# Kernel optimization log

Hardware: AMD Instinct MI355X
Metric: run time of the kernel (lower is better)

The kernel has to match this reference:

```python
import jax, jax.numpy as jnp
import numpy as np

NUM_EXPERTS = 8
TOP_K = 2
IN_C, HID, OUT_C, R_C = 192, 384, 192, 8
B, H, W = 4, 128, 128


def setup_inputs() -> dict:
    key = jax.random.key(0)
    ks = jax.random.split(key, 12)
    s = 0.05
    return {
        "x": jax.random.normal(ks[0], (B, IN_C, H, W), jnp.float32),
        "router_input": jax.random.normal(ks[1], (B, R_C, H, W), jnp.float32),
        "router_W": jax.random.normal(ks[2], (NUM_EXPERTS, R_C), jnp.float32) * s,
        "router_b": jnp.zeros((NUM_EXPERTS,), jnp.float32),
        "W1": jax.random.normal(ks[3], (NUM_EXPERTS, HID, IN_C), jnp.float32) * s,
        "b1": jnp.zeros((NUM_EXPERTS, HID), jnp.float32),
        "W2": jax.random.normal(ks[4], (NUM_EXPERTS, HID, HID), jnp.float32) * s,
        "b2": jnp.zeros((NUM_EXPERTS, HID), jnp.float32),
        "W3": jax.random.normal(ks[5], (NUM_EXPERTS, OUT_C, HID), jnp.float32) * (s * 0.1),
        "b3": jnp.zeros((NUM_EXPERTS, OUT_C), jnp.float32),
    }


def _gates(router_input, router_W, router_b):
    # logits: (B, E, H, W) via 1x1 conv == per-pixel linear
    logits = jnp.einsum('ec,bchw->behw', router_W, router_input) + router_b[None, :, None, None]
    lt = jnp.moveaxis(logits, 1, -1)                      # (B,H,W,E)
    _, idx = jax.lax.top_k(lt, TOP_K)                     # (B,H,W,K)
    onehot = jax.nn.one_hot(idx, NUM_EXPERTS, dtype=bool).any(axis=-2)  # (B,H,W,E)
    masked = jnp.where(onehot, lt, -jnp.inf)
    gates = jax.nn.softmax(masked, axis=-1)               # (B,H,W,E)
    return jnp.moveaxis(gates, -1, 1)                     # (B,E,H,W)


def reference(x, router_input, router_W, router_b, W1, b1, W2, b2, W3, b3):
    gates = _gates(router_input, router_W, router_b)      # (B,E,H,W)
    out = jnp.zeros((x.shape[0], OUT_C) + x.shape[2:], x.dtype)
    gelu = lambda t: jax.nn.gelu(t, approximate=False)    # torch nn.GELU is exact
    for e in range(NUM_EXPERTS):
        h1 = gelu(jnp.einsum('oc,bchw->bohw', W1[e], x) + b1[e][None, :, None, None])
        h2 = gelu(jnp.einsum('oc,bchw->bohw', W2[e], h1) + b2[e][None, :, None, None])
        y = jnp.einsum('oc,bchw->bohw', W3[e], h2) + b3[e][None, :, None, None]
        out = out + gates[:, e:e + 1] * y
    return out
```

## Files before the change

### kernel.cpp

```cpp
#include <hip/hip_runtime.h>
#include <math.h>

#define NE 8
#define IN_C 192
#define HID 384
#define OUT_C 192
#define R_C 8
#define HW 16384
#define NPIX 65536
#define PPB 16384
#define TNP 128

typedef _Float16 h8_t __attribute__((ext_vector_type(8)));
typedef float f32x4 __attribute__((ext_vector_type(4)));

__device__ __forceinline__ float gelu_exact(float v) {
  float z  = v * 0.70710678118654752f;
  float az = fabsf(z);
  float t  = __builtin_amdgcn_rcpf(1.0f + 0.3275911f * az);
  float p  = ((((1.061405429f * t - 1.453152027f) * t + 1.421413741f) * t
               - 0.284496736f) * t + 0.254829592f) * t;
  float er = 1.0f - p * __expf(-z * z);
  er = copysignf(er, z);
  return 0.5f * v * (1.0f + er);
}

__global__ __launch_bounds__(256) void router_kernel(
    const float* __restrict__ rin, const float* __restrict__ rW,
    const float* __restrict__ rb, int* __restrict__ counts,
    int* __restrict__ lists, float* __restrict__ gatev) {
  const int tid = threadIdx.x;
  const int pid = blockIdx.x * 256 + tid;
  const int img = pid >> 14;
  const int p = pid & (PPB - 1);

  __shared__ int lcount[NE];
  __shared__ int lbase[NE];
  if (tid < NE) lcount[tid] = 0;
  __syncthreads();

  const float* rbase = rin + (size_t)img * R_C * HW + p;
  float r[R_C];
#pragma unroll
  for (int c = 0; c < R_C; ++c) r[c] = rbase[(size_t)c * HW];
  float lg[NE];
#pragma unroll
  for (int e = 0; e < NE; ++e) {
    float s = rb[e];
#pragma unroll
    for (int c = 0; c < R_C; ++c) s += rW[e * R_C + c] * r[c];
    lg[e] = s;
  }
  int e0 = 0; float l0 = lg[0];
#pragma unroll
  for (int e = 1; e < NE; ++e) { if (lg[e] > l0) { l0 = lg[e]; e0 = e; } }
  int e1 = -1; float l1 = -3.4e38f;
#pragma unroll
  for (int e = 0; e < NE; ++e) {
    if (e != e0 && lg[e] > l1) { l1 = lg[e]; e1 = e; }
  }
  float ex  = expf(l1 - l0);
  float inv = 1.0f / (1.0f + ex);
  float g0 = inv, g1 = ex * inv;

  int pos0 = atomicAdd(&lcount[e0], 1);
  int pos1 = atomicAdd(&lcount[e1], 1);
  __syncthreads();
  if (tid < NE) lbase[tid] = atomicAdd(&counts[tid * 4 + img], lcount[tid]);
  __syncthreads();

  int i0 = (e0 * 4 + img) * PPB + lbase[e0] + pos0;
  lists[i0] = p;
  gatev[i0] = g0;
  int i1 = (e1 * 4 + img) * PPB + lbase[e1] + pos1;
  lists[i1] = p | (1 << 14);
  gatev[i1] = g1;
}

__global__ __launch_bounds__(256) void cvt_blob(
    const float* __restrict__ W1, const float* __restrict__ W2,
    const float* __restrict__ W3, _Float16* __restrict__ Wb) {
  int t = blockIdx.x * 256 + threadIdx.x;
  if (t >= NE * 73728) return;
  int e = t / 73728, r = t % 73728;
  int cg = r / 1536, w = r % 1536;
  int j4 = w & 1, gm = w >> 1;
  int m = gm % 192, g = gm / 192;
  const float* src; int row, col, lda;
  if (cg < 6)       { src = W1 + (size_t)e * 73728;  row = m;       col = 32 * cg + 8 * g + 4 * j4; lda = 192; }
  else if (cg < 18) { int s = cg - 6;  int c = s >> 1, mh = s & 1;
                      src = W2 + (size_t)e * 147456; row = 192 * mh + m; col = 32 * c + 8 * g + 4 * j4; lda = 384; }
  else if (cg < 24) { int c = cg - 18;
                      src = W1 + (size_t)e * 73728;  row = 192 + m; col = 32 * c + 8 * g + 4 * j4; lda = 192; }
  else if (cg < 36) { int s = cg - 24; int c = s >> 1, mh = s & 1;
                      src = W2 + (size_t)e * 147456; row = 192 * mh + m; col = 192 + 32 * c + 8 * g + 4 * j4; lda = 384; }
  else              { int c = cg - 36;
                      src = W3 + (size_t)e * 73728;  row = m;       col = 32 * c + 8 * g + 4 * j4; lda = 384; }
  float4 v = *(const float4*)(src + (size_t)row * lda + col);
  union { _Float16 h4[4]; uint2 u; } cv;
  cv.h4[0] = (_Float16)v.x; cv.h4[1] = (_Float16)v.y;
  cv.h4[2] = (_Float16)v.z; cv.h4[3] = (_Float16)v.w;
  ((uint2*)Wb)[t] = cv.u;
}

__global__ __launch_bounds__(256) void xt_kernel(const float* __restrict__ x,
                                                 _Float16* __restrict__ xt, int pair) {
  const int img2 = blockIdx.y;
  const float* xb = x + (size_t)(pair * 2 + img2) * IN_C * HW;
  _Float16* dst = xt + (size_t)img2 * PPB * 192;
  const int tid = threadIdx.x;
  const int p = blockIdx.x * 64 + (tid & 63);
  const int cq0 = tid >> 6;
#pragma unroll
  for (int cq = 0; cq < 6; ++cq) {
    int chq = cq * 4 + cq0;
    union { _Float16 h[8]; uint4 u; } pk;
#pragma unroll
    for (int j = 0; j < 8; ++j)
      pk.h[j] = (_Float16)xb[(size_t)(chq * 8 + j) * HW + p];
    *(uint4*)(dst + (size_t)p * 192 + chq * 8) = pk.u;
  }
}

struct Pipe {
  unsigned qi;
  int rslot;
  int cslot;
  const char* wq;
  char* RING;
  int tid, wid;
};

__device__ __forceinline__ void pipe_issue3(Pipe& P) {
#pragma unroll
  for (int k = 0; k < 3; ++k) {
    if (P.qi < 72) {
      __builtin_amdgcn_global_load_lds(
          (const __attribute__((address_space(1))) void*)(P.wq + P.tid * 16),
          (__attribute__((address_space(3))) void*)(P.RING + P.rslot * 8192 + P.wid * 1024),
          16, 0, 0);
      P.wq += 8192;
      P.qi++;
      P.rslot = (P.rslot == 5) ? 0 : P.rslot + 1;
    }
  }
}

__device__ __forceinline__ void mfma_chunk(const _Float16* __restrict__ A,
                                           const _Float16* __restrict__ B, int kb4,
                                           int m0, int nt0,
                                           f32x4 (&acc)[3][4], int lane) {
  const int l15 = lane & 15, g = lane >> 4;
  h8_t a[3], b[4];
#pragma unroll
  for (int i = 0; i < 3; ++i)
    a[i] = *(const h8_t*)(A + ((size_t)g * 192 + m0 + i * 16 + l15) * 8);
#pragma unroll
  for (int t = 0; t < 4; ++t)
    b[t] = *(const h8_t*)(B + (((size_t)(kb4 + g) * TNP) + (nt0 + t) * 16 + l15) * 8);
#pragma unroll
  for (int i = 0; i < 3; ++i)
#pragma unroll
    for (int t = 0; t < 4; ++t)
      acc[i][t] = __builtin_amdgcn_mfma_f32_16x16x32_f16(a[i], b[t], acc[i][t], 0, 0, 0);
}

template <bool LAST, bool DRAIN>
__device__ __forceinline__ void dphase(Pipe& P, const _Float16* __restrict__ Bsh,
                                       int kb0, int kb1,
                                       f32x4 (&accA)[3][4], f32x4 (&accB)[3][4],
                                       int m0loc, int nt0, int lane) {
  if (LAST)       asm volatile("s_waitcnt vmcnt(0)" ::: "memory");
  else if (DRAIN) asm volatile("s_waitcnt vmcnt(3) lgkmcnt(0)" ::: "memory");
  else            asm volatile("s_waitcnt vmcnt(3)" ::: "memory");
  __builtin_amdgcn_sched_barrier(0);
  __builtin_amdgcn_s_barrier();
  __builtin_amdgcn_sched_barrier(0);
  const _Float16* A0 = (const _Float16*)(P.RING + P.cslot * 12288);
  const _Float16* A1 = (const _Float16*)(P.RING + (P.cslot + 1) * 12288);
  __builtin_amdgcn_s_setprio(1);
  mfma_chunk(A0, Bsh, kb0, m0loc, nt0, accA, lane);
  mfma_chunk(A1, Bsh, kb1, m0loc, nt0, accB, lane);
  __builtin_amdgcn_s_setprio(0);
  P.cslot ^= 2;
  if (!LAST) {
    __builtin_amdgcn_sched_barrier(0);
    __builtin_amdgcn_s_barrier();
    __builtin_amdgcn_sched_barrier(0);
    pipe_issue3(P);
  }
}

__device__ __forceinline__ void act_store(f32x4 (&acc)[3][4], const float* __restrict__ bias,
                                          _Float16* __restrict__ Dst, int m0, int nt0, int lane) {
  const int l15 = lane & 15, g = lane >> 4;
#pragma unroll
  for (int i = 0; i < 3; ++i) {
    int rb = m0 + i * 16 + 4 * g;
    float4 bv = *(const float4*)(bias + rb);
#pragma unroll
    for (int t = 0; t < 4; ++t) {
      int n = (nt0 + t) * 16 + l15;
      union { _Float16 h[4]; uint2 u; } cv;
      cv.h[0] = (_Float16)gelu_exact(acc[i][t][0] + bv.x);
      cv.h[1] = (_Float16)gelu_exact(acc[i][t][1] + bv.y);
      cv.h[2] = (_Float16)gelu_exact(acc[i][t][2] + bv.z);
      cv.h[3] = (_Float16)gelu_exact(acc[i][t][3] + bv.w);
      *(uint2*)(Dst + (((size_t)(rb >> 3) * TNP) + n) * 8 + (rb & 7)) = cv.u;
    }
  }
}

__device__ __forceinline__ void ybuf_store(f32x4 (&acc)[3][4], const float* __restrict__ bias,
                                           _Float16* __restrict__ ybuf,
                                           const int* __restrict__ pidsl,
                                           const float* __restrict__ pg,
                                           int npt, int m0, int nt0, int lane) {
  const int l15 = lane & 15, g = lane >> 4;
#pragma unroll
  for (int t = 0; t < 4; ++t) {
    int n = (nt0 + t) * 16 + l15;
    if (n >= npt) continue;
    float gt = pg[n];
    _Float16* yb = ybuf + pidsl[n];
#pragma unroll
    for (int i = 0; i < 3; ++i) {
      int rb = m0 + i * 16 + 4 * g;
      float4 bv = *(const float4*)(bias + rb);
      union { _Float16 h[4]; uint2 u; } cv;
      cv.h[0] = (_Float16)((acc[i][t][0] + bv.x) * gt);
      cv.h[1] = (_Float16)((acc[i][t][1] + bv.y) * gt);
      cv.h[2] = (_Float16)((acc[i][t][2] + bv.z) * gt);
      cv.h[3] = (_Float16)((acc[i][t][3] + bv.w) * gt);
      *(uint2*)(yb + rb) = cv.u;
    }
  }
}

__global__ __launch_bounds__(512, 2) void moe_mfma_kernel(
    const _Float16* __restrict__ xt, const _Float16* __restrict__ Wb,
    const float* __restrict__ b1, const float* __restrict__ b2,
    const float* __restrict__ b3,
    const int* __restrict__ counts, const int* __restrict__ lists,
    const float* __restrict__ gatev, _Float16* __restrict__ ybuf, int pair) {
  const int e = blockIdx.x;
  const int img2 = blockIdx.y >> 7;
  const int tile = blockIdx.y & 127;
  const int img = pair * 2 + img2;
  const int cnt = counts[e * 4 + img];
  const int start = tile * TNP;
  if (start >= cnt) return;
  const int npt = min(TNP, cnt - start);

  __shared__ __align__(16) char smem[152832];
  _Float16* XB  = (_Float16*)smem;
  _Float16* H1a = (_Float16*)(smem + 49152);
  _Float16* H2  = (_Float16*)smem;
  char* RING   = smem + 98304;
  float* BIAS1 = (float*)(smem + 147456);
  float* BIAS2 = (float*)(smem + 148992);
  float* BIAS3 = (float*)(smem + 150528);
  int*   pp    = (int*)(smem + 151296);
  int*   pidsl = (int*)(smem + 151808);
  float* pg    = (float*)(smem + 152320);

  const int tid = threadIdx.x;
  const int lane = tid & 63;
  const int wid = tid >> 6;
  const int m0loc = (wid >> 1) * 48;
  const int nt0 = (wid & 1) * 4;

  if (tid < TNP) {
    int entry = 0; float g = 0.0f;
    if (tid < npt) {
      entry = lists[(e * 4 + img) * PPB + start + tid];
      g     = gatev[(e * 4 + img) * PPB + start + tid];
    }
    int p = entry & (PPB - 1);
    int slot = (entry >> 14) & 1;
    pp[tid] = img2 * PPB + p;
    pidsl[tid] = ((img2 * PPB + p) * 2 + slot) * 192;
    pg[tid] = g;
  }
  for (int i = tid; i < 960; i += 512) {
    if (i < 384) BIAS1[i] = b1[e * HID + i];
    else if (i < 768) BIAS2[i - 384] = b2[e * HID + (i - 384)];
    else BIAS3[i - 768] = b3[e * OUT_C + (i - 768)];
  }
  __syncthreads();

  for (int i = tid; i < 24 * TNP; i += 512) {
    int n = i & (TNP - 1);
    int c16 = i >> 7;
    uint4 v = {0, 0, 0, 0};
    if (n < npt) v = *(const uint4*)(xt + (size_t)pp[n] * 192 + c16 * 8);
    *(uint4*)(XB + ((size_t)c16 * TNP + n) * 8) = v;
  }
  __syncthreads();

  Pipe P{0u, 0, 0, (const char*)(Wb + (size_t)e * 294912), RING, tid, wid};
  pipe_issue3(P);
  pipe_issue3(P);

  f32x4 acc1[3][4], acc2a[3][4], acc2b[3][4];
#pragma unroll
  for (int i = 0; i < 3; ++i)
#pragma unroll
    for (int t = 0; t < 4; ++t) {
      acc1[i][t] = (f32x4){0.f, 0.f, 0.f, 0.f};
      acc2a[i][t] = (f32x4){0.f, 0.f, 0.f, 0.f};
      acc2b[i][t] = (f32x4){0.f, 0.f, 0.f, 0.f};
    }

#pragma unroll 1
  for (int s = 0; s < 3; ++s)
    dphase<false, false>(P, XB, 8 * s, 8 * s + 4, acc1, acc1, m0loc, nt0, lane);
  act_store(acc1, BIAS1, H1a, m0loc, nt0, lane);

  dphase<false, true>(P, H1a, 0, 0, acc2a, acc2b, m0loc, nt0, lane);
#pragma unroll 1
  for (int s = 1; s < 6; ++s)
    dphase<false, false>(P, H1a, 4 * s, 4 * s, acc2a, acc2b, m0loc, nt0, lane);

#pragma unroll
  for (int i = 0; i < 3; ++i)
#pragma unroll
    for (int t = 0; t < 4; ++t) acc1[i][t] = (f32x4){0.f, 0.f, 0.f, 0.f};
#pragma unroll 1
  for (int s = 0; s < 3; ++s)
    dphase<false, false>(P, XB, 8 * s, 8 * s + 4, acc1, acc1, m0loc, nt0, lane);
  act_store(acc1, BIAS1 + 192, H1a, m0loc, nt0, lane);

  dphase<false, true>(P, H1a, 0, 0, acc2a, acc2b, m0loc, nt0, lane);
#pragma unroll 1
  for (int s = 1; s < 6; ++s)
    dphase<false, false>(P, H1a, 4 * s, 4 * s, acc2a, acc2b, m0loc, nt0, lane);
  act_store(acc2a, BIAS2, H2, m0loc, nt0, lane);
  act_store(acc2b, BIAS2, H2, 192 + m0loc, nt0, lane);

#pragma unroll
  for (int i = 0; i < 3; ++i)
#pragma unroll
    for (int t = 0; t < 4; ++t) acc1[i][t] = (f32x4){0.f, 0.f, 0.f, 0.f};
  dphase<false, true>(P, H2, 0, 4, acc1, acc1, m0loc, nt0, lane);
#pragma unroll 1
  for (int s = 1; s < 5; ++s)
    dphase<false, false>(P, H2, 8 * s, 8 * s + 4, acc1, acc1, m0loc, nt0, lane);
  dphase<true, false>(P, H2, 40, 44, acc1, acc1, m0loc, nt0, lane);

  ybuf_store(acc1, BIAS3, ybuf, pidsl, pg, npt, m0loc, nt0, lane);
}

__global__ __launch_bounds__(256) void sum_kernel(
    const _Float16* __restrict__ ybuf, float* __restrict__ out, int pair) {
  __shared__ float ys[64][193];
  const int tid = threadIdx.x;
  const int img2 = blockIdx.x >> 8;
  const int p0 = (blockIdx.x & 255) * 64;
  const _Float16* yb = ybuf + (size_t)(img2 * PPB + p0) * 2 * 192;

  for (int t = tid; t < 64 * 48; t += 256) {
    int p = t / 48, c4 = t % 48;
    const uint2* y0 = (const uint2*)(yb + (size_t)p * 2 * 192) + c4;
    uint2 u0 = y0[0];
    uint2 u1 = y0[48];
    union { uint2 u; _Float16 h[4]; } a, b;
    a.u = u0; b.u = u1;
#pragma unroll
    for (int j = 0; j < 4; ++j)
      ys[p][c4 * 4 + j] = (float)a.h[j] + (float)b.h[j];
  }
  __syncthreads();

  float* ob = out + (size_t)(pair * 2 + img2) * OUT_C * HW + p0;
  for (int t = tid; t < OUT_C * 64; t += 256) {
    int c = t >> 6, p = t & 63;
    ob[(size_t)c * HW + p] = ys[p][c];
  }
}

extern "C" void kernel_launch(void* const* d_in, const int* in_sizes, int n_in,
                              void* d_out, int out_size, void* d_ws, size_t ws_size,
                              hipStream_t stream) {
  const float* x   = (const float*)d_in[0];
  const float* rin = (const float*)d_in[1];
  const float* rW  = (const float*)d_in[2];
  const float* rb  = (const float*)d_in[3];
  const float* W1  = (const float*)d_in[4];
  const float* b1  = (const float*)d_in[5];
  const float* W2  = (const float*)d_in[6];
  const float* b2  = (const float*)d_in[7];
  const float* W3  = (const float*)d_in[8];
  const float* b3  = (const float*)d_in[9];
  float* out = (float*)d_out;

  char* ws = (char*)d_ws;
  int*   counts = (int*)ws;
  int*   lists  = (int*)(ws + 1024);
  float* gatev  = (float*)(ws + 1024 + (size_t)NE * 4 * PPB * 4);
  _Float16* Wb  = (_Float16*)(ws + 1024 + 2 * (size_t)NE * 4 * PPB * 4);
  _Float16* ybuf = Wb + (size_t)NE * 294912;
  _Float16* xt = ybuf + (size_t)2 * PPB * 2 * 192;

  hipMemsetAsync(counts, 0, NE * 4 * sizeof(int), stream);

  cvt_blob<<<(NE * 73728 + 255) / 256, 256, 0, stream>>>(W1, W2, W3, Wb);

  router_kernel<<<NPIX / 256, 256, 0, stream>>>(rin, rW, rb, counts, lists, gatev);

  for (int pair = 0; pair < 2; ++pair) {
    xt_kernel<<<dim3(PPB / 64, 2), 256, 0, stream>>>(x, xt, pair);
    moe_mfma_kernel<<<dim3(NE, 256), 512, 0, stream>>>(
        xt, Wb, b1, b2, b3, counts, lists, gatev, ybuf, pair);
    sum_kernel<<<512, 256, 0, stream>>>(ybuf, out, pair);
  }
}
```

Measured before the change: 262.6 us.

## Halve pixel tile to 64 and use a double-buffered weight pipeline

The per-block pixel tile drops from 128 to 64, which halves shared memory (to about 78 KB) and the accumulator registers so more blocks fit per CU (launch bounds raised to 4). The 6-slot weight ring with 3-chunk issue is replaced by a simpler 2-slot double buffer of 12 KB chunks, with fully unrolled per-stage loops and explicit wait counts. The trade-off is that each weight chunk streamed from L2 is now reused across only half as many pixels, so weight traffic per pixel doubles, and the shallower prefetch depth leaves less latency hiding.

```diff
diff --git a/kernel.cpp b/kernel.cpp
--- a/kernel.cpp
+++ b/kernel.cpp
@@ -9,7 +9,7 @@
 #define HW 16384
 #define NPIX 65536
 #define PPB 16384
-#define TNP 128
+#define TNP 64
 
 typedef _Float16 h8_t __attribute__((ext_vector_type(8)));
 typedef float f32x4 __attribute__((ext_vector_type(4)));
@@ -122,76 +122,48 @@
   }
 }
 
-struct Pipe {
-  unsigned qi;
-  int rslot;
-  int cslot;
-  const char* wq;
-  char* RING;
-  int tid, wid;
-};
-
-__device__ __forceinline__ void pipe_issue3(Pipe& P) {
-#pragma unroll
-  for (int k = 0; k < 3; ++k) {
-    if (P.qi < 72) {
-      __builtin_amdgcn_global_load_lds(
-          (const __attribute__((address_space(1))) void*)(P.wq + P.tid * 16),
-          (__attribute__((address_space(3))) void*)(P.RING + P.rslot * 8192 + P.wid * 1024),
-          16, 0, 0);
-      P.wq += 8192;
-      P.qi++;
-      P.rslot = (P.rslot == 5) ? 0 : P.rslot + 1;
-    }
-  }
-}
-
-__device__ __forceinline__ void mfma_chunk(const _Float16* __restrict__ A,
-                                           const _Float16* __restrict__ B, int kb4,
-                                           int m0, int nt0,
-                                           f32x4 (&acc)[3][4], int lane) {
-  const int l15 = lane & 15, g = lane >> 4;
-  h8_t a[3], b[4];
+__device__ __forceinline__ void stage_chunk(const char* __restrict__ g,
+                                            char* lds, int tid, int wid) {
+  __builtin_amdgcn_global_load_lds(
+      (const __attribute__((address_space(1))) void*)(g + tid * 16),
+      (__attribute__((address_space(3))) void*)(lds + wid * 1024), 16, 0, 0);
+  if (wid < 4)
+    __builtin_amdgcn_global_load_lds(
+        (const __attribute__((address_space(1))) void*)(g + 8192 + tid * 16),
+        (__attribute__((address_space(3))) void*)(lds + 8192 + wid * 1024), 16, 0, 0);
+}
+
+__device__ __forceinline__ void pwait_c(int wid, bool last) {
+  if (last)         asm volatile("s_waitcnt vmcnt(0)" ::: "memory");
+  else if (wid < 4) asm volatile("s_waitcnt vmcnt(2)" ::: "memory");
+  else              asm volatile("s_waitcnt vmcnt(1)" ::: "memory");
+  __builtin_amdgcn_s_barrier();
+  __builtin_amdgcn_sched_barrier(0);
+}
+
+__device__ __forceinline__ void read_B2(const _Float16* __restrict__ Bsh, int kb4,
+                                        int nt0, int l15, int g, h8_t (&b)[2]) {
+#pragma unroll
+  for (int t = 0; t < 2; ++t)
+    b[t] = *(const h8_t*)(Bsh + (((size_t)(kb4 + g) * TNP) + (nt0 + t) * 16 + l15) * 8);
+}
+
+__device__ __forceinline__ void mfma32(const _Float16* __restrict__ A, const h8_t (&b)[2],
+                                       int m0, f32x4 (&acc)[3][2], int l15, int g) {
+  h8_t a[3];
 #pragma unroll
   for (int i = 0; i < 3; ++i)
     a[i] = *(const h8_t*)(A + ((size_t)g * 192 + m0 + i * 16 + l15) * 8);
-#pragma unroll
-  for (int t = 0; t < 4; ++t)
-    b[t] = *(const h8_t*)(B + (((size_t)(kb4 + g) * TNP) + (nt0 + t) * 16 + l15) * 8);
+  __builtin_amdgcn_s_setprio(1);
 #pragma unroll
   for (int i = 0; i < 3; ++i)
 #pragma unroll
-    for (int t = 0; t < 4; ++t)
+    for (int t = 0; t < 2; ++t)
       acc[i][t] = __builtin_amdgcn_mfma_f32_16x16x32_f16(a[i], b[t], acc[i][t], 0, 0, 0);
-}
-
-template <bool LAST, bool DRAIN>
-__device__ __forceinline__ void dphase(Pipe& P, const _Float16* __restrict__ Bsh,
-                                       int kb0, int kb1,
-                                       f32x4 (&accA)[3][4], f32x4 (&accB)[3][4],
-                                       int m0loc, int nt0, int lane) {
-  if (LAST)       asm volatile("s_waitcnt vmcnt(0)" ::: "memory");
-  else if (DRAIN) asm volatile("s_waitcnt vmcnt(3) lgkmcnt(0)" ::: "memory");
-  else            asm volatile("s_waitcnt vmcnt(3)" ::: "memory");
-  __builtin_amdgcn_sched_barrier(0);
-  __builtin_amdgcn_s_barrier();
-  __builtin_amdgcn_sched_barrier(0);
-  const _Float16* A0 = (const _Float16*)(P.RING + P.cslot * 12288);
-  const _Float16* A1 = (const _Float16*)(P.RING + (P.cslot + 1) * 12288);
-  __builtin_amdgcn_s_setprio(1);
-  mfma_chunk(A0, Bsh, kb0, m0loc, nt0, accA, lane);
-  mfma_chunk(A1, Bsh, kb1, m0loc, nt0, accB, lane);
   __builtin_amdgcn_s_setprio(0);
-  P.cslot ^= 2;
-  if (!LAST) {
-    __builtin_amdgcn_sched_barrier(0);
-    __builtin_amdgcn_s_barrier();
-    __builtin_amdgcn_sched_barrier(0);
-    pipe_issue3(P);
-  }
-}
-
-__device__ __forceinline__ void act_store(f32x4 (&acc)[3][4], const float* __restrict__ bias,
+}
+
+__device__ __forceinline__ void act_store(f32x4 (&acc)[3][2], const float* __restrict__ bias,
                                           _Float16* __restrict__ Dst, int m0, int nt0, int lane) {
   const int l15 = lane & 15, g = lane >> 4;
 #pragma unroll
@@ -199,7 +171,7 @@
     int rb = m0 + i * 16 + 4 * g;
     float4 bv = *(const float4*)(bias + rb);
 #pragma unroll
-    for (int t = 0; t < 4; ++t) {
+    for (int t = 0; t < 2; ++t) {
       int n = (nt0 + t) * 16 + l15;
       union { _Float16 h[4]; uint2 u; } cv;
       cv.h[0] = (_Float16)gelu_exact(acc[i][t][0] + bv.x);
@@ -211,14 +183,14 @@
   }
 }
 
-__device__ __forceinline__ void ybuf_store(f32x4 (&acc)[3][4], const float* __restrict__ bias,
+__device__ __forceinline__ void ybuf_store(f32x4 (&acc)[3][2], const float* __restrict__ bias,
                                            _Float16* __restrict__ ybuf,
                                            const int* __restrict__ pidsl,
                                            const float* __restrict__ pg,
                                            int npt, int m0, int nt0, int lane) {
   const int l15 = lane & 15, g = lane >> 4;
 #pragma unroll
-  for (int t = 0; t < 4; ++t) {
+  for (int t = 0; t < 2; ++t) {
     int n = (nt0 + t) * 16 + l15;
     if (n >= npt) continue;
     float gt = pg[n];
@@ -237,50 +209,52 @@
   }
 }
 
-__global__ __launch_bounds__(512, 2) void moe_mfma_kernel(
+__global__ __launch_bounds__(512, 4) void moe_mfma_kernel(
     const _Float16* __restrict__ xt, const _Float16* __restrict__ Wb,
     const float* __restrict__ b1, const float* __restrict__ b2,
     const float* __restrict__ b3,
     const int* __restrict__ counts, const int* __restrict__ lists,
     const float* __restrict__ gatev, _Float16* __restrict__ ybuf, int pair) {
   const int e = blockIdx.x;
-  const int img2 = blockIdx.y >> 7;
-  const int tile = blockIdx.y & 127;
+  const int img2 = blockIdx.y >> 8;
+  const int tile = blockIdx.y & 255;
   const int img = pair * 2 + img2;
   const int cnt = counts[e * 4 + img];
   const int start = tile * TNP;
   if (start >= cnt) return;
   const int npt = min(TNP, cnt - start);
 
-  __shared__ __align__(16) char smem[152832];
+  __shared__ __align__(16) char smem[78336];
   _Float16* XB  = (_Float16*)smem;
-  _Float16* H1a = (_Float16*)(smem + 49152);
+  _Float16* H1a = (_Float16*)(smem + 24576);
   _Float16* H2  = (_Float16*)smem;
-  char* RING   = smem + 98304;
-  float* BIAS1 = (float*)(smem + 147456);
-  float* BIAS2 = (float*)(smem + 148992);
-  float* BIAS3 = (float*)(smem + 150528);
-  int*   pp    = (int*)(smem + 151296);
-  int*   pidsl = (int*)(smem + 151808);
-  float* pg    = (float*)(smem + 152320);
+  char* RING   = smem + 49152;
+  float* BIAS1 = (float*)(smem + 73728);
+  float* BIAS2 = (float*)(smem + 75264);
+  float* BIAS3 = (float*)(smem + 76800);
+  int*   pp    = (int*)(smem + 77568);
+  int*   pidsl = (int*)(smem + 77824);
+  float* pg    = (float*)(smem + 78080);
 
   const int tid = threadIdx.x;
   const int lane = tid & 63;
   const int wid = tid >> 6;
+  const int l15 = lane & 15;
+  const int g = lane >> 4;
   const int m0loc = (wid >> 1) * 48;
-  const int nt0 = (wid & 1) * 4;
+  const int nt0 = (wid & 1) * 2;
 
   if (tid < TNP) {
-    int entry = 0; float g = 0.0f;
+    int entry = 0; float gt = 0.0f;
     if (tid < npt) {
       entry = lists[(e * 4 + img) * PPB + start + tid];
-      g     = gatev[(e * 4 + img) * PPB + start + tid];
+      gt    = gatev[(e * 4 + img) * PPB + start + tid];
     }
     int p = entry & (PPB - 1);
     int slot = (entry >> 14) & 1;
     pp[tid] = img2 * PPB + p;
     pidsl[tid] = ((img2 * PPB + p) * 2 + slot) * 192;
-    pg[tid] = g;
+    pg[tid] = gt;
   }
   for (int i = tid; i < 960; i += 512) {
     if (i < 384) BIAS1[i] = b1[e * HID + i];
@@ -291,62 +265,108 @@
 
   for (int i = tid; i < 24 * TNP; i += 512) {
     int n = i & (TNP - 1);
-    int c16 = i >> 7;
+    int c16 = i >> 6;
     uint4 v = {0, 0, 0, 0};
     if (n < npt) v = *(const uint4*)(xt + (size_t)pp[n] * 192 + c16 * 8);
     *(uint4*)(XB + ((size_t)c16 * TNP + n) * 8) = v;
   }
   __syncthreads();
 
-  Pipe P{0u, 0, 0, (const char*)(Wb + (size_t)e * 294912), RING, tid, wid};
-  pipe_issue3(P);
-  pipe_issue3(P);
-
-  f32x4 acc1[3][4], acc2a[3][4], acc2b[3][4];
+  const char* blob = (const char*)(Wb + (size_t)e * 294912);
+  stage_chunk(blob, RING, tid, wid);
+  stage_chunk(blob + 12288, RING + 12288, tid, wid);
+
+  f32x4 acc1[3][2], acc2a[3][2], acc2b[3][2];
 #pragma unroll
   for (int i = 0; i < 3; ++i)
 #pragma unroll
-    for (int t = 0; t < 4; ++t) {
+    for (int t = 0; t < 2; ++t) {
       acc1[i][t] = (f32x4){0.f, 0.f, 0.f, 0.f};
       acc2a[i][t] = (f32x4){0.f, 0.f, 0.f, 0.f};
       acc2b[i][t] = (f32x4){0.f, 0.f, 0.f, 0.f};
     }
 
-#pragma unroll 1
-  for (int s = 0; s < 3; ++s)
-    dphase<false, false>(P, XB, 8 * s, 8 * s + 4, acc1, acc1, m0loc, nt0, lane);
-  act_store(acc1, BIAS1, H1a, m0loc, nt0, lane);
-
-  dphase<false, true>(P, H1a, 0, 0, acc2a, acc2b, m0loc, nt0, lane);
-#pragma unroll 1
-  for (int s = 1; s < 6; ++s)
-    dphase<false, false>(P, H1a, 4 * s, 4 * s, acc2a, acc2b, m0loc, nt0, lane);
+  h8_t b[2];
+
+#pragma unroll
+  for (int s = 0; s < 6; ++s) {
+    pwait_c(wid, false);
+    read_B2(XB, 4 * s, nt0, l15, g, b);
+    mfma32((const _Float16*)(RING + (s & 1) * 12288), b, m0loc, acc1, l15, g);
+    if (s == 5) {
+      act_store(acc1, BIAS1, H1a, m0loc, nt0, lane);
+      asm volatile("s_waitcnt lgkmcnt(0)");
+    }
+    __builtin_amdgcn_sched_barrier(0);
+    __builtin_amdgcn_s_barrier();
+    __builtin_amdgcn_sched_barrier(0);
+    stage_chunk(blob + (size_t)(s + 2) * 12288, RING + (s & 1) * 12288, tid, wid);
+  }
+
+#pragma unroll
+  for (int s = 0; s < 12; ++s) {
+    pwait_c(wid, false);
+    if ((s & 1) == 0) read_B2(H1a, 4 * (s >> 1), nt0, l15, g, b);
+    mfma32((const _Float16*)(RING + (s & 1) * 12288), b, m0loc,
+           (s & 1) ? acc2b : acc2a, l15, g);
+    __builtin_amdgcn_sched_barrier(0);
+    __builtin_amdgcn_s_barrier();
+    __builtin_amdgcn_sched_barrier(0);
+    stage_chunk(blob + (size_t)(s + 8) * 12288, RING + (s & 1) * 12288, tid, wid);
+  }
 
 #pragma unroll
   for (int i = 0; i < 3; ++i)
 #pragma unroll
-    for (int t = 0; t < 4; ++t) acc1[i][t] = (f32x4){0.f, 0.f, 0.f, 0.f};
-#pragma unroll 1
-  for (int s = 0; s < 3; ++s)
-    dphase<false, false>(P, XB, 8 * s, 8 * s + 4, acc1, acc1, m0loc, nt0, lane);
-  act_store(acc1, BIAS1 + 192, H1a, m0loc, nt0, lane);
-
-  dphase<false, true>(P, H1a, 0, 0, acc2a, acc2b, m0loc, nt0, lane);
-#pragma unroll 1
-  for (int s = 1; s < 6; ++s)
-    dphase<false, false>(P, H1a, 4 * s, 4 * s, acc2a, acc2b, m0loc, nt0, lane);
-  act_store(acc2a, BIAS2, H2, m0loc, nt0, lane);
-  act_store(acc2b, BIAS2, H2, 192 + m0loc, nt0, lane);
+    for (int t = 0; t < 2; ++t) acc1[i][t] = (f32x4){0.f, 0.f, 0.f, 0.f};
+#pragma unroll
+  for (int s = 0; s < 6; ++s) {
+    pwait_c(wid, false);
+    read_B2(XB, 4 * s, nt0, l15, g, b);
+    mfma32((const _Float16*)(RING + (s & 1) * 12288), b, m0loc, acc1, l15, g);
+    if (s == 5) {
+      act_store(acc1, BIAS1 + 192, H1a, m0loc, nt0, lane);
+      asm volatile("s_waitcnt lgkmcnt(0)");
+    }
+    __builtin_amdgcn_sched_barrier(0);
+    __builtin_amdgcn_s_barrier();
+    __builtin_amdgcn_sched_barrier(0);
+    stage_chunk(blob + (size_t)(s + 20) * 12288, RING + (s & 1) * 12288, tid, wid);
+  }
+
+#pragma unroll
+  for (int s = 0; s < 12; ++s) {
+    pwait_c(wid, false);
+    if ((s & 1) == 0) read_B2(H1a, 4 * (s >> 1), nt0, l15, g, b);
+    mfma32((const _Float16*)(RING + (s & 1) * 12288), b, m0loc,
+           (s & 1) ? acc2b : acc2a, l15, g);
+    if (s == 11) {
+      act_store(acc2a, BIAS2, H2, m0loc, nt0, lane);
+      act_store(acc2b, BIAS2, H2, 192 + m0loc, nt0, lane);
+      asm volatile("s_waitcnt lgkmcnt(0)");
+    }
+    __builtin_amdgcn_sched_barrier(0);
+    __builtin_amdgcn_s_barrier();
+    __builtin_amdgcn_sched_barrier(0);
+    stage_chunk(blob + (size_t)(s + 26) * 12288, RING + (s & 1) * 12288, tid, wid);
+  }
 
 #pragma unroll
   for (int i = 0; i < 3; ++i)
 #pragma unroll
-    for (int t = 0; t < 4; ++t) acc1[i][t] = (f32x4){0.f, 0.f, 0.f, 0.f};
-  dphase<false, true>(P, H2, 0, 4, acc1, acc1, m0loc, nt0, lane);
-#pragma unroll 1
-  for (int s = 1; s < 5; ++s)
-    dphase<false, false>(P, H2, 8 * s, 8 * s + 4, acc1, acc1, m0loc, nt0, lane);
-  dphase<true, false>(P, H2, 40, 44, acc1, acc1, m0loc, nt0, lane);
+    for (int t = 0; t < 2; ++t) acc1[i][t] = (f32x4){0.f, 0.f, 0.f, 0.f};
+#pragma unroll
+  for (int s = 0; s < 12; ++s) {
+    pwait_c(wid, s == 11);
+    read_B2(H2, 4 * s, nt0, l15, g, b);
+    mfma32((const _Float16*)(RING + (s & 1) * 12288), b, m0loc, acc1, l15, g);
+    if (s < 10) {
+      __builtin_amdgcn_sched_barrier(0);
+      __builtin_amdgcn_s_barrier();
+      __builtin_amdgcn_sched_barrier(0);
+      stage_chunk(blob + (size_t)(s + 38) * 12288, RING + (s & 1) * 12288, tid, wid);
+    }
+  }
 
   ybuf_store(acc1, BIAS3, ybuf, pidsl, pg, npt, m0loc, nt0, lane);
 }
@@ -410,7 +430,7 @@
 
   for (int pair = 0; pair < 2; ++pair) {
     xt_kernel<<<dim3(PPB / 64, 2), 256, 0, stream>>>(x, xt, pair);
-    moe_mfma_kernel<<<dim3(NE, 256), 512, 0, stream>>>(
+    moe_mfma_kernel<<<dim3(NE, 512), 512, 0, stream>>>(
         xt, Wb, b1, b2, b3, counts, lists, gatev, ybuf, pair);
     sum_kernel<<<512, 256, 0, stream>>>(ybuf, out, pair);
   }
```

Result: faster. 239.9 us, median of 2 (-8.6%).
